# Performance work log

Hardware: AMD Instinct MI355X
Metric: run time of the kernel (lower is better)

Reference implementation:

```python
import jax, jax.numpy as jnp
import numpy as np

EMB = 1024
HEADS = 16
HEAD_DIM = EMB // HEADS
EPS = 1e-5


def gelu_tanh(x):
    c = jnp.sqrt(jnp.asarray(2.0 / jnp.pi, x.dtype))
    return 0.5 * x * (1 + jnp.tanh(c * (x + 0.044715 * x ** 3)))


def layernorm(x, scale, shift):
    mean = jnp.mean(x, axis=-1, keepdims=True)
    var = jnp.mean((x - mean) ** 2, axis=-1, keepdims=True)
    return scale * (x - mean) / jnp.sqrt(var + EPS) + shift


def setup_inputs() -> dict:
    key = jax.random.key(0)
    ks = jax.random.split(key, 12)
    s = 0.02
    x = jax.random.normal(ks[0], (2, 2048, EMB), dtype=jnp.float32)
    Wq = jax.random.normal(ks[1], (EMB, EMB), dtype=jnp.float32) * s
    Wk = jax.random.normal(ks[2], (EMB, EMB), dtype=jnp.float32) * s
    Wv = jax.random.normal(ks[3], (EMB, EMB), dtype=jnp.float32) * s
    Wo = jax.random.normal(ks[4], (EMB, EMB), dtype=jnp.float32) * s
    bo = jnp.zeros((EMB,), jnp.float32)
    W1 = jax.random.normal(ks[5], (EMB, 4 * EMB), dtype=jnp.float32) * s
    b1 = jnp.zeros((4 * EMB,), jnp.float32)
    W2 = jax.random.normal(ks[6], (4 * EMB, EMB), dtype=jnp.float32) * s
    b2 = jnp.zeros((EMB,), jnp.float32)
    g1 = jnp.ones((EMB,), jnp.float32)
    s1 = jnp.zeros((EMB,), jnp.float32)
    g2 = jnp.ones((EMB,), jnp.float32)
    s2 = jnp.zeros((EMB,), jnp.float32)
    return {"x": x, "Wq": Wq, "Wk": Wk, "Wv": Wv, "Wo": Wo, "bo": bo,
            "W1": W1, "b1": b1, "W2": W2, "b2": b2,
            "g1": g1, "s1": s1, "g2": g2, "s2": s2}


def reference(x, Wq, Wk, Wv, Wo, bo, W1, b1, W2, b2, g1, s1, g2, s2):
    B, S, D = x.shape
    # --- attention sub-block (pre-LN) ---
    h = layernorm(x, g1, s1)
    q = (h @ Wq).reshape(B, S, HEADS, HEAD_DIM).transpose(0, 2, 1, 3)
    k = (h @ Wk).reshape(B, S, HEADS, HEAD_DIM).transpose(0, 2, 1, 3)
    v = (h @ Wv).reshape(B, S, HEADS, HEAD_DIM).transpose(0, 2, 1, 3)
    scores = jnp.einsum('bhqd,bhkd->bhqk', q, k) / jnp.sqrt(
        jnp.asarray(HEAD_DIM, x.dtype))
    causal = jnp.triu(jnp.ones((S, S), bool), k=1)
    scores = jnp.where(causal, -jnp.inf, scores)
    attn = jax.nn.softmax(scores, axis=-1)
    ctx = jnp.einsum('bhqk,bhkd->bhqd', attn, v)
    ctx = ctx.transpose(0, 2, 1, 3).reshape(B, S, D)
    x = x + (ctx @ Wo + bo)
    # --- FFN sub-block (pre-LN) ---
    h = layernorm(x, g2, s2)
    h = gelu_tanh(h @ W1 + b1) @ W2 + b2
    return x + h
```

## Files before the change

kernel.cpp:

```cpp
#include <hip/hip_runtime.h>
#include <hip/hip_bf16.h>
#include <math.h>
#include <stdint.h>

typedef __bf16 bf16;
typedef __bf16 bf16x4 __attribute__((ext_vector_type(4)));
typedef __bf16 bf16x8 __attribute__((ext_vector_type(8)));
typedef float f32x4 __attribute__((ext_vector_type(4)));

#define MFMA16(a, b, c) __builtin_amdgcn_mfma_f32_16x16x32_bf16((a), (b), (c), 0, 0, 0)

constexpr int EMB = 1024;
constexpr int SEQ = 2048;
constexpr int BATCH = 2;
constexpr int NTOK = BATCH * SEQ;
constexpr int FFN = 4 * EMB;
constexpr int HEADS = 16;
constexpr int HDIM = 64;

#define QSCALE 0.18033688011112042f

__device__ __forceinline__ void gload16(const void* g, void* l) {
    __builtin_amdgcn_global_load_lds(
        (const __attribute__((address_space(1))) void*)g,
        (__attribute__((address_space(3))) void*)l,
        16, 0, 0);
}

__global__ __launch_bounds__(256) void ln_kernel(const float* __restrict__ x,
                                                 const float* __restrict__ g,
                                                 const float* __restrict__ b,
                                                 bf16* __restrict__ out) {
    int row = blockIdx.x;
    int t = threadIdx.x;
    float4 v = reinterpret_cast<const float4*>(x + (size_t)row * EMB)[t];
    float s = v.x + v.y + v.z + v.w;
    float s2 = v.x * v.x + v.y * v.y + v.z * v.z + v.w * v.w;
#pragma unroll
    for (int o = 1; o < 64; o <<= 1) {
        s += __shfl_xor(s, o);
        s2 += __shfl_xor(s2, o);
    }
    __shared__ float ps[4], ps2[4];
    int w = t >> 6;
    if ((t & 63) == 0) { ps[w] = s; ps2[w] = s2; }
    __syncthreads();
    s = ps[0] + ps[1] + ps[2] + ps[3];
    s2 = ps2[0] + ps2[1] + ps2[2] + ps2[3];
    float mean = s * (1.f / EMB);
    float var = s2 * (1.f / EMB) - mean * mean;
    float rstd = rsqrtf(var + 1e-5f);
    float4 gv = reinterpret_cast<const float4*>(g)[t];
    float4 bv = reinterpret_cast<const float4*>(b)[t];
    bf16* op = out + (size_t)row * EMB + t * 4;
    op[0] = (bf16)(gv.x * (v.x - mean) * rstd + bv.x);
    op[1] = (bf16)(gv.y * (v.y - mean) * rstd + bv.y);
    op[2] = (bf16)(gv.z * (v.z - mean) * rstd + bv.z);
    op[3] = (bf16)(gv.w * (v.w - mean) * rstd + bv.w);
}

__global__ __launch_bounds__(256) void transpose_all(
    const float* __restrict__ Wq, const float* __restrict__ Wk,
    const float* __restrict__ Wv, const float* __restrict__ Wo,
    const float* __restrict__ W1, const float* __restrict__ W2,
    bf16* __restrict__ Wqkvt, bf16* __restrict__ Wot,
    bf16* __restrict__ W1t, bf16* __restrict__ W2t) {
    int b = blockIdx.x;
    const float* W;
    bf16* Wt;
    int K, N, tile;
    if (b < 4096) {
        int w = b >> 10;
        tile = b & 1023;
        W = (w == 0) ? Wq : (w == 1) ? Wk : (w == 2) ? Wv : Wo;
        Wt = (w == 3) ? Wot : Wqkvt + (size_t)w * EMB * EMB;
        K = EMB; N = EMB;
    } else if (b < 8192) {
        tile = b - 4096; W = W1; Wt = W1t; K = EMB; N = FFN;
    } else {
        tile = b - 8192; W = W2; Wt = W2t; K = FFN; N = EMB;
    }
    int ntx = N / 32;
    int n0 = (tile % ntx) * 32, k0 = (tile / ntx) * 32;
    __shared__ float tl[32][33];
    int tx = threadIdx.x & 31, ty = threadIdx.x >> 5;
#pragma unroll
    for (int i = 0; i < 4; i++)
        tl[ty + 8 * i][tx] = W[(size_t)(k0 + ty + 8 * i) * N + n0 + tx];
    __syncthreads();
#pragma unroll
    for (int i = 0; i < 4; i++)
        Wt[(size_t)(n0 + ty + 8 * i) * K + k0 + tx] = (bf16)tl[tx][ty + 8 * i];
}

__global__ __launch_bounds__(256) void vtrans(const bf16* __restrict__ v,
                                              bf16* __restrict__ vt) {
    int bh = blockIdx.y;
    int s0 = blockIdx.x * 64;
    const bf16* src = v + (size_t)bh * SEQ * HDIM + (size_t)s0 * HDIM;
    bf16* dst = vt + (size_t)bh * HDIM * SEQ + s0;
    __shared__ bf16 tile[64][72];
    int t = threadIdx.x;
    int s = t >> 2, d0 = (t & 3) * 16;
    bf16x8 a = *reinterpret_cast<const bf16x8*>(src + s * HDIM + d0);
    bf16x8 b = *reinterpret_cast<const bf16x8*>(src + s * HDIM + d0 + 8);
#pragma unroll
    for (int e = 0; e < 8; e++) {
        tile[d0 + e][s] = a[e];
        tile[d0 + 8 + e][s] = b[e];
    }
    __syncthreads();
    int d = t >> 2, c0 = (t & 3) * 16;
    bf16x8 o0 = *reinterpret_cast<const bf16x8*>(&tile[d][c0]);
    bf16x8 o1 = *reinterpret_cast<const bf16x8*>(&tile[d][c0 + 8]);
    *reinterpret_cast<bf16x8*>(dst + (size_t)d * SEQ + c0) = o0;
    *reinterpret_cast<bf16x8*>(dst + (size_t)d * SEQ + c0 + 8) = o1;
}

template <int MODE>
__global__ __launch_bounds__(512, 1) void gemm8p(const bf16* __restrict__ A,
                                                 const bf16* __restrict__ Bt,
                                                 int K, int N,
                                                 bf16* __restrict__ outB,
                                                 bf16* __restrict__ outB2,
                                                 const float* __restrict__ bias) {
    extern __shared__ char smem[];
    int t = threadIdx.x;
    int wave = t >> 6, lane = t & 63;
    int wr = wave >> 2, wc = wave & 3;
    int lr = lane & 15, lg = lane >> 4;
    int row0 = blockIdx.x * 256;
    int col0 = blockIdx.y * 256;

    int tilesAll = K / 64;
    int nz = gridDim.z, z = blockIdx.z;
    int base = tilesAll / nz, rem = tilesAll - base * nz;
    int myT = base + (z < rem ? 1 : 0);
    int tBeg = z * base + (z < rem ? z : rem);

    const char* aSrc[4];
    const char* bSrc[4];
#pragma unroll
    for (int i = 0; i < 4; i++) {
        int f = t + i * 512;
        int gr = f >> 3, gk = f & 7;
        aSrc[i] = (const char*)A + ((size_t)(row0 + gr) * K + ((gk ^ (gr & 7)) << 3)) * 2
                  + (size_t)tBeg * 128;
        bSrc[i] = (const char*)Bt + ((size_t)(col0 + gr) * K + ((gk ^ (gr & 7)) << 3)) * 2
                  + (size_t)tBeg * 128;
    }

    f32x4 acc[8][4];
#pragma unroll
    for (int m = 0; m < 8; m++)
#pragma unroll
        for (int n = 0; n < 4; n++) acc[m][n] = f32x4{0.f, 0.f, 0.f, 0.f};

#pragma unroll
    for (int i = 0; i < 4; i++) {
        gload16(aSrc[i], smem + (t + i * 512) * 16);
        gload16(bSrc[i], smem + 32768 + (t + i * 512) * 16);
    }
    __syncthreads();

    for (int tk = 0; tk < myT; tk++) {
        int cur = tk & 1;
        const char* la = smem + cur * 65536;
        const char* lb = la + 32768;
        char* na = smem + (cur ^ 1) * 65536;
        bool stage = (tk + 1 < myT);

        bf16x8 bfr[2][4];
#pragma unroll
        for (int ph = 0; ph < 4; ph++) {
            constexpr int PH_KH[4] = {0, 0, 1, 1};
            constexpr int PH_MH[4] = {0, 1, 0, 1};
            const int kh = PH_KH[ph], mh = PH_MH[ph];
            bf16x8 afr[4];
#pragma unroll
            for (int m = 0; m < 4; m++) {
                int row = wr * 128 + (mh * 4 + m) * 16 + lr;
                int gk = kh * 4 + lg;
                afr[m] = *reinterpret_cast<const bf16x8*>(
                    la + row * 128 + ((gk ^ (row & 7)) << 4));
            }
            if (mh == 0) {
#pragma unroll
                for (int n = 0; n < 4; n++) {
                    int row = wc * 64 + n * 16 + lr;
                    int gk = kh * 4 + lg;
                    bfr[kh][n] = *reinterpret_cast<const bf16x8*>(
                        lb + row * 128 + ((gk ^ (row & 7)) << 4));
                }
            }
            if (stage) {
                gload16(aSrc[ph] + 128, na + (t + ph * 512) * 16);
                gload16(bSrc[ph] + 128, na + 32768 + (t + ph * 512) * 16);
            }
            __builtin_amdgcn_s_barrier();
            __builtin_amdgcn_s_setprio(1);
#pragma unroll
            for (int m = 0; m < 4; m++)
#pragma unroll
                for (int n = 0; n < 4; n++)
                    acc[mh * 4 + m][n] = MFMA16(afr[m], bfr[kh][n], acc[mh * 4 + m][n]);
            __builtin_amdgcn_s_setprio(0);
            __builtin_amdgcn_s_barrier();
        }
#pragma unroll
        for (int i = 0; i < 4; i++) { aSrc[i] += 128; bSrc[i] += 128; }
        __syncthreads();
    }

    float bi[4];
    if (MODE == 2) {
#pragma unroll
        for (int n = 0; n < 4; n++) bi[n] = bias[col0 + wc * 64 + n * 16 + lr];
    }
    bf16* pd = outB;
    if (MODE == 3) pd = (z < 2) ? outB + (size_t)z * ((size_t)NTOK * EMB) : outB2;
#pragma unroll
    for (int mf = 0; mf < 8; mf++) {
#pragma unroll
        for (int r = 0; r < 4; r++) {
            int row = row0 + wr * 128 + mf * 16 + 4 * lg + r;
#pragma unroll
            for (int n = 0; n < 4; n++) {
                int col = col0 + wc * 64 + n * 16 + lr;
                float v = acc[mf][n][r];
                if (MODE == 0) {
                    int b_ = row >> 11, s_ = row & 2047;
                    int which = col >> 10, rem_ = col & 1023;
                    int h_ = rem_ >> 6, d_ = rem_ & 63;
                    float sc = (which == 0) ? QSCALE : 1.0f;
                    outB[(size_t)which * (NTOK * EMB) +
                         (((size_t)(b_ * HEADS + h_) * SEQ + s_) << 6) + d_] =
                        (bf16)(v * sc);
                } else if (MODE == 2) {
                    float u = v + bi[n];
                    float gl = 0.5f * u *
                               (1.f + tanhf(0.7978845608028654f *
                                            (u + 0.044715f * u * u * u)));
                    outB[(size_t)row * N + col] = (bf16)gl;
                } else {
                    pd[(size_t)row * N + col] = (bf16)v;
                }
            }
        }
    }
}

__global__ __launch_bounds__(256) void ffn2_reduce(const float* __restrict__ x1,
                                                   const bf16* __restrict__ p01,
                                                   const bf16* __restrict__ p2,
                                                   const float* __restrict__ bias,
                                                   float* __restrict__ out) {
    constexpr int UNITS = NTOK * EMB / 4;
    const bf16* p1 = p01 + (size_t)NTOK * EMB;
    for (int i = blockIdx.x * 256 + threadIdx.x; i < UNITS; i += gridDim.x * 256) {
        float4 r = reinterpret_cast<const float4*>(x1)[i];
        float4 bv = reinterpret_cast<const float4*>(bias)[i & (EMB / 4 - 1)];
        bf16x4 a0 = reinterpret_cast<const bf16x4*>(p01)[i];
        bf16x4 a1 = reinterpret_cast<const bf16x4*>(p1)[i];
        bf16x4 a2 = reinterpret_cast<const bf16x4*>(p2)[i];
        r.x += (float)a0[0] + (float)a1[0] + (float)a2[0] + bv.x;
        r.y += (float)a0[1] + (float)a1[1] + (float)a2[1] + bv.y;
        r.z += (float)a0[2] + (float)a1[2] + (float)a2[2] + bv.z;
        r.w += (float)a0[3] + (float)a1[3] + (float)a2[3] + bv.w;
        reinterpret_cast<float4*>(out)[i] = r;
    }
}

template <int BM, int BN, int BK, int MODE>
__global__ __launch_bounds__(256) void gemm_lds(const bf16* __restrict__ A,
                                                const bf16* __restrict__ Bt,
                                                int M, int N, int K,
                                                float* __restrict__ outF,
                                                bf16* __restrict__ outB,
                                                const float* __restrict__ bias,
                                                const float* __restrict__ resid) {
    constexpr int MR = BM / 32;
    constexpr int NR = BN / 32;
    constexpr int ACH = (BM * BK * 2) / 4096;
    constexpr int BCH = (BN * BK * 2) / 4096;
    __shared__ bf16 sA[BM * BK];
    __shared__ bf16 sB[BN * BK];
    int t = threadIdx.x;
    int wave = t >> 6, lane = t & 63;
    int wr = wave >> 1, wc = wave & 1;
    int lr = lane & 15, lg = lane >> 4;
    int row0 = blockIdx.x * BM;
    int col0 = blockIdx.y * BN;

    const char* aS[ACH];
    const char* bS[BCH];
#pragma unroll
    for (int c = 0; c < ACH; c++) {
        int o = (t + c * 256) * 16;
        aS[c] = (const char*)A + (size_t)(row0 + o / (2 * BK)) * K * 2 + (o & (2 * BK - 1));
    }
#pragma unroll
    for (int c = 0; c < BCH; c++) {
        int o = (t + c * 256) * 16;
        bS[c] = (const char*)Bt + (size_t)(col0 + o / (2 * BK)) * K * 2 + (o & (2 * BK - 1));
    }

    f32x4 acc[MR][NR];
#pragma unroll
    for (int m = 0; m < MR; m++)
#pragma unroll
        for (int n = 0; n < NR; n++) acc[m][n] = f32x4{0.f, 0.f, 0.f, 0.f};

    for (int k0 = 0; k0 < K; k0 += BK) {
        __syncthreads();
#pragma unroll
        for (int c = 0; c < ACH; c++)
            gload16(aS[c], (char*)sA + (t + c * 256) * 16);
#pragma unroll
        for (int c = 0; c < BCH; c++)
            gload16(bS[c], (char*)sB + (t + c * 256) * 16);
#pragma unroll
        for (int c = 0; c < ACH; c++) aS[c] += 2 * BK;
#pragma unroll
        for (int c = 0; c < BCH; c++) bS[c] += 2 * BK;
        __syncthreads();

#pragma unroll
        for (int ks = 0; ks < BK / 32; ks++) {
            bf16x8 a[MR], b[NR];
#pragma unroll
            for (int m = 0; m < MR; m++)
                a[m] = *reinterpret_cast<const bf16x8*>(
                    sA + (wr * (BM / 2) + m * 16 + lr) * BK + ks * 32 + 8 * lg);
#pragma unroll
            for (int n = 0; n < NR; n++)
                b[n] = *reinterpret_cast<const bf16x8*>(
                    sB + (wc * (BN / 2) + n * 16 + lr) * BK + ks * 32 + 8 * lg);
#pragma unroll
            for (int m = 0; m < MR; m++)
#pragma unroll
                for (int n = 0; n < NR; n++)
                    acc[m][n] = MFMA16(a[m], b[n], acc[m][n]);
        }
    }

#pragma unroll
    for (int m = 0; m < MR; m++) {
#pragma unroll
        for (int r = 0; r < 4; r++) {
            int row = row0 + wr * (BM / 2) + m * 16 + 4 * lg + r;
#pragma unroll
            for (int n = 0; n < NR; n++) {
                int col = col0 + wc * (BN / 2) + n * 16 + lr;
                float v = acc[m][n][r];
                size_t idx = (size_t)row * N + col;
                outF[idx] = resid[idx] + v + bias[col];
            }
        }
    }
}

__global__ __launch_bounds__(256, 3) void attn_kernel(const bf16* __restrict__ q,
                                                      const bf16* __restrict__ k,
                                                      const bf16* __restrict__ vt,
                                                      bf16* __restrict__ ctx) {
    int wg = blockIdx.x;
    int wgid = (wg & 7) * 64 + (wg >> 3);
    int bh = wgid >> 4;
    int pair = wgid & 15;
    const bf16* qh = q + (size_t)bh * SEQ * HDIM;
    const bf16* kh = k + (size_t)bh * SEQ * HDIM;
    const bf16* vh = vt + (size_t)bh * HDIM * SEQ;
    int t = threadIdx.x;
    int wave = t >> 6, lane = t & 63;
    int lr = lane & 15, lg = lane >> 4;

    __shared__ bf16 sK[2][64 * 64];
    __shared__ bf16 sV[2][64 * 64];
    __shared__ bf16 plds[4][16][88];

    int grow = t >> 3, gg = t & 7;
    const bf16* kSrc0 = kh + (size_t)grow * HDIM + ((gg ^ (grow & 7)) << 3);
    const bf16* kSrc1 = kh + (size_t)(grow + 32) * HDIM + ((gg ^ ((grow + 32) & 7)) << 3);
    const bf16* vSrc0 = vh + (size_t)grow * SEQ + ((gg ^ (grow & 7)) << 3);
    const bf16* vSrc1 = vh + (size_t)(grow + 32) * SEQ + ((gg ^ ((grow + 32) & 7)) << 3);
    char* kD0 = (char*)&sK[0][0] + wave * 1024;
    char* vD0 = (char*)&sV[0][0] + wave * 1024;

    int swz = (lr & 7) << 4;
    int koff0 = (16 * lg) ^ swz;
    int koff1 = (64 + 16 * lg) ^ swz;
    int b_ = bh >> 4, h_ = bh & 15;

    for (int seg = 0; seg < 2; seg++) {
        int q0 = (seg == 0 ? (31 - pair) : pair) * 64;
        int qrow = q0 + wave * 16;

        bf16x8 qf0 = *reinterpret_cast<const bf16x8*>(
            qh + (size_t)(qrow + lr) * HDIM + 8 * lg);
        bf16x8 qf1 = *reinterpret_cast<const bf16x8*>(
            qh + (size_t)(qrow + lr) * HDIM + 32 + 8 * lg);

        f32x4 o[4];
#pragma unroll
        for (int n = 0; n < 4; n++) o[n] = f32x4{0.f, 0.f, 0.f, 0.f};
        float mx[4] = {-1e30f, -1e30f, -1e30f, -1e30f};
        float lsum[4] = {0.f, 0.f, 0.f, 0.f};

        int nc = q0 / 64 + 1;

        gload16(kSrc0, kD0);
        gload16(kSrc1, kD0 + 4096);
        gload16(vSrc0, vD0);
        gload16(vSrc1, vD0 + 4096);
        __syncthreads();

        for (int c = 0; c < nc; c++) {
            int c0 = c * 64;
            if (c + 1 < nc) {
                int nb = (c + 1) & 1;
                int cn = c0 + 64;
                gload16(kSrc0 + (size_t)cn * HDIM, kD0 + nb * 8192);
                gload16(kSrc1 + (size_t)cn * HDIM, kD0 + nb * 8192 + 4096);
                gload16(vSrc0 + cn, vD0 + nb * 8192);
                gload16(vSrc1 + cn, vD0 + nb * 8192 + 4096);
            }
            const char* kb_ = (const char*)&sK[c & 1][0];
            const char* vb_ = (const char*)&sV[c & 1][0];

            f32x4 st[4];
#pragma unroll
            for (int n = 0; n < 4; n++) {
                int ro = (16 * n + lr) * 128;
                bf16x8 kf0 = *reinterpret_cast<const bf16x8*>(kb_ + ro + koff0);
                bf16x8 kf1 = *reinterpret_cast<const bf16x8*>(kb_ + ro + koff1);
                f32x4 a = f32x4{0.f, 0.f, 0.f, 0.f};
                a = MFMA16(qf0, kf0, a);
                a = MFMA16(qf1, kf1, a);
                st[n] = a;
            }

            if (c0 == q0) {
#pragma unroll
                for (int n = 0; n < 4; n++)
#pragma unroll
                    for (int r = 0; r < 4; r++)
                        if (c0 + n * 16 + lr > qrow + 4 * lg + r) st[n][r] = -1e30f;
            }

            float mn[4], scl[4], ps[4];
#pragma unroll
            for (int r = 0; r < 4; r++) {
                float mp = fmaxf(fmaxf(st[0][r], st[1][r]), fmaxf(st[2][r], st[3][r]));
#pragma unroll
                for (int off = 1; off < 16; off <<= 1)
                    mp = fmaxf(mp, __shfl_xor(mp, off));
                mn[r] = fmaxf(mx[r], mp);
                scl[r] = __builtin_amdgcn_exp2f(mx[r] - mn[r]);
                mx[r] = mn[r];
                ps[r] = 0.f;
            }
#pragma unroll
            for (int n = 0; n < 4; n++)
#pragma unroll
                for (int r = 0; r < 4; r++) {
                    float p = __builtin_amdgcn_exp2f(st[n][r] - mn[r]);
                    ps[r] += p;
                    plds[wave][4 * lg + r][n * 16 + lr] = (bf16)p;
                }
#pragma unroll
            for (int r = 0; r < 4; r++) {
                float s = ps[r];
#pragma unroll
                for (int off = 1; off < 16; off <<= 1) s += __shfl_xor(s, off);
                lsum[r] = lsum[r] * scl[r] + s;
            }
#pragma unroll
            for (int n = 0; n < 4; n++) {
                o[n][0] *= scl[0]; o[n][1] *= scl[1];
                o[n][2] *= scl[2]; o[n][3] *= scl[3];
            }

#pragma unroll
            for (int ks = 0; ks < 2; ks++) {
                bf16x8 pa = *reinterpret_cast<const bf16x8*>(
                    &plds[wave][lr][ks * 32 + 8 * lg]);
                int vo = (64 * ks + 16 * lg) ^ swz;
#pragma unroll
                for (int n = 0; n < 4; n++) {
                    bf16x8 vf = *reinterpret_cast<const bf16x8*>(
                        vb_ + (16 * n + lr) * 128 + vo);
                    o[n] = MFMA16(pa, vf, o[n]);
                }
            }

            __syncthreads();
        }

#pragma unroll
        for (int r = 0; r < 4; r++) {
            float inv = 1.f / lsum[r];
            size_t base = ((size_t)b_ * SEQ + qrow + 4 * lg + r) * EMB + h_ * HDIM;
#pragma unroll
            for (int n = 0; n < 4; n++)
                ctx[base + n * 16 + lr] = (bf16)(o[n][r] * inv);
        }
    }
}

extern "C" void kernel_launch(void* const* d_in, const int* in_sizes, int n_in,
                              void* d_out, int out_size, void* d_ws, size_t ws_size,
                              hipStream_t stream) {
    const float* x  = (const float*)d_in[0];
    const float* Wq = (const float*)d_in[1];
    const float* Wk = (const float*)d_in[2];
    const float* Wv = (const float*)d_in[3];
    const float* Wo = (const float*)d_in[4];
    const float* bo = (const float*)d_in[5];
    const float* W1 = (const float*)d_in[6];
    const float* b1 = (const float*)d_in[7];
    const float* W2 = (const float*)d_in[8];
    const float* b2 = (const float*)d_in[9];
    const float* g1 = (const float*)d_in[10];
    const float* s1 = (const float*)d_in[11];
    const float* g2 = (const float*)d_in[12];
    const float* s2 = (const float*)d_in[13];

    const size_t MB = 1ull << 20;
    char* w = (char*)d_ws;
    bf16* Wqkvt = (bf16*)(w + 0 * MB);
    bf16* Wot = (bf16*)(w + 6 * MB);
    bf16* W1t = (bf16*)(w + 8 * MB);
    bf16* W2t = (bf16*)(w + 16 * MB);
    bf16* hbuf = (bf16*)(w + 24 * MB);
    bf16* vtb  = (bf16*)(w + 24 * MB);
    bf16* qkvb = (bf16*)(w + 32 * MB);
    bf16* qb   = (bf16*)(w + 32 * MB);
    bf16* kb   = (bf16*)(w + 40 * MB);
    bf16* vb   = (bf16*)(w + 48 * MB);
    bf16* ctxb = (bf16*)(w + 56 * MB);
    bf16* midb = (bf16*)(w + 32 * MB);
    float* x1  = (float*)(w + 64 * MB);
    bf16* p01  = (bf16*)(w + 0 * MB);
    bf16* p2   = (bf16*)(w + 24 * MB);

    hipFuncSetAttribute(reinterpret_cast<const void*>(gemm8p<0>),
                        hipFuncAttributeMaxDynamicSharedMemorySize, 131072);
    hipFuncSetAttribute(reinterpret_cast<const void*>(gemm8p<2>),
                        hipFuncAttributeMaxDynamicSharedMemorySize, 131072);
    hipFuncSetAttribute(reinterpret_cast<const void*>(gemm8p<3>),
                        hipFuncAttributeMaxDynamicSharedMemorySize, 131072);

    transpose_all<<<dim3(12288), 256, 0, stream>>>(Wq, Wk, Wv, Wo, W1, W2,
                                                   Wqkvt, Wot, W1t, W2t);

    ln_kernel<<<NTOK, 256, 0, stream>>>(x, g1, s1, hbuf);

    gemm8p<0><<<dim3(NTOK / 256, 3072 / 256), 512, 131072, stream>>>(
        hbuf, Wqkvt, EMB, 3072, qkvb, nullptr, nullptr);

    vtrans<<<dim3(SEQ / 64, BATCH * HEADS), 256, 0, stream>>>(vb, vtb);

    attn_kernel<<<dim3(512), 256, 0, stream>>>(qb, kb, vtb, ctxb);

    gemm_lds<128, 64, 32, 1><<<dim3(NTOK / 128, EMB / 64), 256, 0, stream>>>(
        ctxb, Wot, NTOK, EMB, EMB, x1, nullptr, bo, x);

    ln_kernel<<<NTOK, 256, 0, stream>>>(x1, g2, s2, hbuf);

    gemm8p<2><<<dim3(NTOK / 256, FFN / 256), 512, 131072, stream>>>(
        hbuf, W1t, EMB, FFN, midb, nullptr, b1);

    gemm8p<3><<<dim3(NTOK / 256, EMB / 256, 3), 512, 131072, stream>>>(
        midb, W2t, FFN, EMB, p01, p2, nullptr);
    ffn2_reduce<<<dim3(2048), 256, 0, stream>>>(x1, p01, p2, b2, (float*)d_out);
}
```

Measured before the change: 255.5 us.

## Process both causal query tiles concurrently in one 512-thread attention block

The attention kernel now uses 512 threads. The two paired query tiles (pair and 31-pair) are handled at the same time by the two halves of the block, instead of one after the other. Each K/V chunk is loaded into shared memory once and reused by both halves, and the early-finishing half simply idles through the remaining chunks. This removes the second pass's reloading of K/V chunks and the serial segment loop. In exchange, the shorter half's waves sit idle at the barriers, and the larger block may lower occupancy per CU.

```diff
diff --git a/kernel.cpp b/kernel.cpp
--- a/kernel.cpp
+++ b/kernel.cpp
@@ -360,7 +360,7 @@
     }
 }
 
-__global__ __launch_bounds__(256, 3) void attn_kernel(const bf16* __restrict__ q,
+__global__ __launch_bounds__(512, 2) void attn_kernel(const bf16* __restrict__ q,
                                                       const bf16* __restrict__ k,
                                                       const bf16* __restrict__ vt,
                                                       bf16* __restrict__ ctx) {
@@ -375,56 +375,52 @@
     int wave = t >> 6, lane = t & 63;
     int lr = lane & 15, lg = lane >> 4;
 
+    int half = wave >> 2;
+    int q0 = (half ? pair : (31 - pair)) * 64;
+    int qrow = q0 + (wave & 3) * 16;
+    int myNc = q0 / 64 + 1;
+    int ncAll = 32 - pair;
+
     __shared__ bf16 sK[2][64 * 64];
     __shared__ bf16 sV[2][64 * 64];
-    __shared__ bf16 plds[4][16][88];
+    __shared__ bf16 plds[8][16][88];
 
     int grow = t >> 3, gg = t & 7;
-    const bf16* kSrc0 = kh + (size_t)grow * HDIM + ((gg ^ (grow & 7)) << 3);
-    const bf16* kSrc1 = kh + (size_t)(grow + 32) * HDIM + ((gg ^ ((grow + 32) & 7)) << 3);
-    const bf16* vSrc0 = vh + (size_t)grow * SEQ + ((gg ^ (grow & 7)) << 3);
-    const bf16* vSrc1 = vh + (size_t)(grow + 32) * SEQ + ((gg ^ ((grow + 32) & 7)) << 3);
-    char* kD0 = (char*)&sK[0][0] + wave * 1024;
-    char* vD0 = (char*)&sV[0][0] + wave * 1024;
+    const bf16* kSrc = kh + (size_t)grow * HDIM + ((gg ^ (grow & 7)) << 3);
+    const bf16* vSrc = vh + (size_t)grow * SEQ + ((gg ^ (grow & 7)) << 3);
+    char* kD = (char*)&sK[0][0] + wave * 1024;
+    char* vD = (char*)&sV[0][0] + wave * 1024;
 
     int swz = (lr & 7) << 4;
     int koff0 = (16 * lg) ^ swz;
     int koff1 = (64 + 16 * lg) ^ swz;
     int b_ = bh >> 4, h_ = bh & 15;
 
-    for (int seg = 0; seg < 2; seg++) {
-        int q0 = (seg == 0 ? (31 - pair) : pair) * 64;
-        int qrow = q0 + wave * 16;
-
-        bf16x8 qf0 = *reinterpret_cast<const bf16x8*>(
-            qh + (size_t)(qrow + lr) * HDIM + 8 * lg);
-        bf16x8 qf1 = *reinterpret_cast<const bf16x8*>(
-            qh + (size_t)(qrow + lr) * HDIM + 32 + 8 * lg);
-
-        f32x4 o[4];
-#pragma unroll
-        for (int n = 0; n < 4; n++) o[n] = f32x4{0.f, 0.f, 0.f, 0.f};
-        float mx[4] = {-1e30f, -1e30f, -1e30f, -1e30f};
-        float lsum[4] = {0.f, 0.f, 0.f, 0.f};
-
-        int nc = q0 / 64 + 1;
-
-        gload16(kSrc0, kD0);
-        gload16(kSrc1, kD0 + 4096);
-        gload16(vSrc0, vD0);
-        gload16(vSrc1, vD0 + 4096);
-        __syncthreads();
-
-        for (int c = 0; c < nc; c++) {
-            int c0 = c * 64;
-            if (c + 1 < nc) {
-                int nb = (c + 1) & 1;
-                int cn = c0 + 64;
-                gload16(kSrc0 + (size_t)cn * HDIM, kD0 + nb * 8192);
-                gload16(kSrc1 + (size_t)cn * HDIM, kD0 + nb * 8192 + 4096);
-                gload16(vSrc0 + cn, vD0 + nb * 8192);
-                gload16(vSrc1 + cn, vD0 + nb * 8192 + 4096);
-            }
+    bf16x8 qf0 = *reinterpret_cast<const bf16x8*>(
+        qh + (size_t)(qrow + lr) * HDIM + 8 * lg);
+    bf16x8 qf1 = *reinterpret_cast<const bf16x8*>(
+        qh + (size_t)(qrow + lr) * HDIM + 32 + 8 * lg);
+
+    f32x4 o[4];
+#pragma unroll
+    for (int n = 0; n < 4; n++) o[n] = f32x4{0.f, 0.f, 0.f, 0.f};
+    float mx[4] = {-1e30f, -1e30f, -1e30f, -1e30f};
+    float lsum[4] = {0.f, 0.f, 0.f, 0.f};
+
+    gload16(kSrc, kD);
+    gload16(vSrc, vD);
+    __syncthreads();
+
+    for (int c = 0; c < ncAll; c++) {
+        int c0 = c * 64;
+        if (c + 1 < ncAll) {
+            int nb = (c + 1) & 1;
+            int cn = c0 + 64;
+            gload16(kSrc + (size_t)cn * HDIM, kD + nb * 8192);
+            gload16(vSrc + cn, vD + nb * 8192);
+        }
+
+        if (c < myNc) {
             const char* kb_ = (const char*)&sK[c & 1][0];
             const char* vb_ = (const char*)&sV[c & 1][0];
 
@@ -493,18 +489,18 @@
                     o[n] = MFMA16(pa, vf, o[n]);
                 }
             }
-
-            __syncthreads();
         }
 
-#pragma unroll
-        for (int r = 0; r < 4; r++) {
-            float inv = 1.f / lsum[r];
-            size_t base = ((size_t)b_ * SEQ + qrow + 4 * lg + r) * EMB + h_ * HDIM;
-#pragma unroll
-            for (int n = 0; n < 4; n++)
-                ctx[base + n * 16 + lr] = (bf16)(o[n][r] * inv);
-        }
+        __syncthreads();
+    }
+
+#pragma unroll
+    for (int r = 0; r < 4; r++) {
+        float inv = 1.f / lsum[r];
+        size_t base = ((size_t)b_ * SEQ + qrow + 4 * lg + r) * EMB + h_ * HDIM;
+#pragma unroll
+        for (int n = 0; n < 4; n++)
+            ctx[base + n * 16 + lr] = (bf16)(o[n][r] * inv);
     }
 }
 
@@ -561,7 +557,7 @@
 
     vtrans<<<dim3(SEQ / 64, BATCH * HEADS), 256, 0, stream>>>(vb, vtb);
 
-    attn_kernel<<<dim3(512), 256, 0, stream>>>(qb, kb, vtb, ctxb);
+    attn_kernel<<<dim3(512), 512, 0, stream>>>(qb, kb, vtb, ctxb);
 
     gemm_lds<128, 64, 32, 1><<<dim3(NTOK / 128, EMB / 64), 256, 0, stream>>>(
         ctxb, Wot, NTOK, EMB, EMB, x1, nullptr, bo, x);
```

Result: no change. 256.8 us (+0.5%).

## Rewrite attention with 32x32 MFMA, transposed scores, and single-pass paired query tiles

Applied to the files above, without the earlier changes.

The attention kernel moves from 16x16x32 to 32x32x16 bf16 MFMA and computes transposed score tiles (K as the A operand), so each lane owns one query row and the softmax reductions need only one cross-lane shuffle. The two sequential causal segments become one pass: waves 0-1 take the long query tile and waves 2-3 the short one, sharing a single K/V stream over the longer range. The goal is fewer instructions, less shuffle and LDS traffic per score, and reuse of shared K/V loads. In exchange, the short-tile waves sit idle for the remaining chunks while still hitting barriers, and 32x32 accumulators raise register pressure.

```diff
diff --git a/kernel.cpp b/kernel.cpp
--- a/kernel.cpp
+++ b/kernel.cpp
@@ -7,8 +7,10 @@
 typedef __bf16 bf16x4 __attribute__((ext_vector_type(4)));
 typedef __bf16 bf16x8 __attribute__((ext_vector_type(8)));
 typedef float f32x4 __attribute__((ext_vector_type(4)));
+typedef float f32x16 __attribute__((ext_vector_type(16)));
 
 #define MFMA16(a, b, c) __builtin_amdgcn_mfma_f32_16x16x32_bf16((a), (b), (c), 0, 0, 0)
+#define MFMA32(a, b, c) __builtin_amdgcn_mfma_f32_32x32x16_bf16((a), (b), (c), 0, 0, 0)
 
 constexpr int EMB = 1024;
 constexpr int SEQ = 2048;
@@ -373,11 +375,16 @@
     const bf16* vh = vt + (size_t)bh * HDIM * SEQ;
     int t = threadIdx.x;
     int wave = t >> 6, lane = t & 63;
-    int lr = lane & 15, lg = lane >> 4;
+    int ql = lane & 31, hi = lane >> 5;
+
+    int span = (wave < 2 ? (31 - pair) : pair) * 64;
+    int qrow = span + (wave & 1) * 32;
+    int myNc = span / 64 + 1;
+    int ncAll = 32 - pair;
 
     __shared__ bf16 sK[2][64 * 64];
     __shared__ bf16 sV[2][64 * 64];
-    __shared__ bf16 plds[4][16][88];
+    __shared__ bf16 plds[4][32][72];
 
     int grow = t >> 3, gg = t & 7;
     const bf16* kSrc0 = kh + (size_t)grow * HDIM + ((gg ^ (grow & 7)) << 3);
@@ -387,124 +394,116 @@
     char* kD0 = (char*)&sK[0][0] + wave * 1024;
     char* vD0 = (char*)&sV[0][0] + wave * 1024;
 
-    int swz = (lr & 7) << 4;
-    int koff0 = (16 * lg) ^ swz;
-    int koff1 = (64 + 16 * lg) ^ swz;
     int b_ = bh >> 4, h_ = bh & 15;
 
-    for (int seg = 0; seg < 2; seg++) {
-        int q0 = (seg == 0 ? (31 - pair) : pair) * 64;
-        int qrow = q0 + wave * 16;
-
-        bf16x8 qf0 = *reinterpret_cast<const bf16x8*>(
-            qh + (size_t)(qrow + lr) * HDIM + 8 * lg);
-        bf16x8 qf1 = *reinterpret_cast<const bf16x8*>(
-            qh + (size_t)(qrow + lr) * HDIM + 32 + 8 * lg);
-
-        f32x4 o[4];
-#pragma unroll
-        for (int n = 0; n < 4; n++) o[n] = f32x4{0.f, 0.f, 0.f, 0.f};
-        float mx[4] = {-1e30f, -1e30f, -1e30f, -1e30f};
-        float lsum[4] = {0.f, 0.f, 0.f, 0.f};
-
-        int nc = q0 / 64 + 1;
-
-        gload16(kSrc0, kD0);
-        gload16(kSrc1, kD0 + 4096);
-        gload16(vSrc0, vD0);
-        gload16(vSrc1, vD0 + 4096);
-        __syncthreads();
-
-        for (int c = 0; c < nc; c++) {
-            int c0 = c * 64;
-            if (c + 1 < nc) {
-                int nb = (c + 1) & 1;
-                int cn = c0 + 64;
-                gload16(kSrc0 + (size_t)cn * HDIM, kD0 + nb * 8192);
-                gload16(kSrc1 + (size_t)cn * HDIM, kD0 + nb * 8192 + 4096);
-                gload16(vSrc0 + cn, vD0 + nb * 8192);
-                gload16(vSrc1 + cn, vD0 + nb * 8192 + 4096);
-            }
+    bf16x8 qf[4];
+#pragma unroll
+    for (int ks = 0; ks < 4; ks++)
+        qf[ks] = *reinterpret_cast<const bf16x8*>(
+            qh + (size_t)(qrow + ql) * HDIM + ks * 16 + 8 * hi);
+
+    f32x16 o0, o1;
+#pragma unroll
+    for (int r = 0; r < 16; r++) { o0[r] = 0.f; o1[r] = 0.f; }
+    float mx = -1e30f, lsum = 0.f;
+
+    gload16(kSrc0, kD0);
+    gload16(kSrc1, kD0 + 4096);
+    gload16(vSrc0, vD0);
+    gload16(vSrc1, vD0 + 4096);
+    __syncthreads();
+
+    for (int c = 0; c < ncAll; c++) {
+        int c0 = c * 64;
+        if (c + 1 < ncAll) {
+            int nb = (c + 1) & 1;
+            int cn = c0 + 64;
+            gload16(kSrc0 + (size_t)cn * HDIM, kD0 + nb * 8192);
+            gload16(kSrc1 + (size_t)cn * HDIM, kD0 + nb * 8192 + 4096);
+            gload16(vSrc0 + cn, vD0 + nb * 8192);
+            gload16(vSrc1 + cn, vD0 + nb * 8192 + 4096);
+        }
+
+        if (c < myNc) {
             const char* kb_ = (const char*)&sK[c & 1][0];
             const char* vb_ = (const char*)&sV[c & 1][0];
 
-            f32x4 st[4];
-#pragma unroll
-            for (int n = 0; n < 4; n++) {
-                int ro = (16 * n + lr) * 128;
-                bf16x8 kf0 = *reinterpret_cast<const bf16x8*>(kb_ + ro + koff0);
-                bf16x8 kf1 = *reinterpret_cast<const bf16x8*>(kb_ + ro + koff1);
-                f32x4 a = f32x4{0.f, 0.f, 0.f, 0.f};
-                a = MFMA16(qf0, kf0, a);
-                a = MFMA16(qf1, kf1, a);
-                st[n] = a;
-            }
-
-            if (c0 == q0) {
-#pragma unroll
-                for (int n = 0; n < 4; n++)
-#pragma unroll
-                    for (int r = 0; r < 4; r++)
-                        if (c0 + n * 16 + lr > qrow + 4 * lg + r) st[n][r] = -1e30f;
-            }
-
-            float mn[4], scl[4], ps[4];
-#pragma unroll
-            for (int r = 0; r < 4; r++) {
-                float mp = fmaxf(fmaxf(st[0][r], st[1][r]), fmaxf(st[2][r], st[3][r]));
-#pragma unroll
-                for (int off = 1; off < 16; off <<= 1)
-                    mp = fmaxf(mp, __shfl_xor(mp, off));
-                mn[r] = fmaxf(mx[r], mp);
-                scl[r] = __builtin_amdgcn_exp2f(mx[r] - mn[r]);
-                mx[r] = mn[r];
-                ps[r] = 0.f;
-            }
-#pragma unroll
-            for (int n = 0; n < 4; n++)
-#pragma unroll
-                for (int r = 0; r < 4; r++) {
-                    float p = __builtin_amdgcn_exp2f(st[n][r] - mn[r]);
-                    ps[r] += p;
-                    plds[wave][4 * lg + r][n * 16 + lr] = (bf16)p;
+            f32x16 st0, st1;
+#pragma unroll
+            for (int r = 0; r < 16; r++) { st0[r] = 0.f; st1[r] = 0.f; }
+#pragma unroll
+            for (int ks = 0; ks < 4; ks++) {
+                int so = ((2 * ks + hi) ^ (ql & 7)) << 4;
+                bf16x8 kA0 = *reinterpret_cast<const bf16x8*>(kb_ + ql * 128 + so);
+                bf16x8 kA1 = *reinterpret_cast<const bf16x8*>(kb_ + (32 + ql) * 128 + so);
+                st0 = MFMA32(kA0, qf[ks], st0);
+                st1 = MFMA32(kA1, qf[ks], st1);
+            }
+
+            if (c == myNc - 1) {
+#pragma unroll
+                for (int r = 0; r < 16; r++) {
+                    int kl = c0 + (r & 3) + 8 * (r >> 2) + 4 * hi;
+                    if (kl > qrow + ql) st0[r] = -1e30f;
+                    if (kl + 32 > qrow + ql) st1[r] = -1e30f;
                 }
-#pragma unroll
-            for (int r = 0; r < 4; r++) {
-                float s = ps[r];
-#pragma unroll
-                for (int off = 1; off < 16; off <<= 1) s += __shfl_xor(s, off);
-                lsum[r] = lsum[r] * scl[r] + s;
-            }
-#pragma unroll
-            for (int n = 0; n < 4; n++) {
-                o[n][0] *= scl[0]; o[n][1] *= scl[1];
-                o[n][2] *= scl[2]; o[n][3] *= scl[3];
-            }
-
-#pragma unroll
-            for (int ks = 0; ks < 2; ks++) {
-                bf16x8 pa = *reinterpret_cast<const bf16x8*>(
-                    &plds[wave][lr][ks * 32 + 8 * lg]);
-                int vo = (64 * ks + 16 * lg) ^ swz;
-#pragma unroll
-                for (int n = 0; n < 4; n++) {
-                    bf16x8 vf = *reinterpret_cast<const bf16x8*>(
-                        vb_ + (16 * n + lr) * 128 + vo);
-                    o[n] = MFMA16(pa, vf, o[n]);
+            }
+
+            float pmax = -1e30f;
+#pragma unroll
+            for (int r = 0; r < 16; r++)
+                pmax = fmaxf(pmax, fmaxf(st0[r], st1[r]));
+            pmax = fmaxf(pmax, __shfl_xor(pmax, 32));
+            float mn = fmaxf(mx, pmax);
+            float scl = __builtin_amdgcn_exp2f(mx - mn);
+            mx = mn;
+            float ps = 0.f;
+#pragma unroll
+            for (int j = 0; j < 4; j++) {
+                bf16x4 w0, w1;
+#pragma unroll
+                for (int e = 0; e < 4; e++) {
+                    float p0 = __builtin_amdgcn_exp2f(st0[4 * j + e] - mn);
+                    float p1 = __builtin_amdgcn_exp2f(st1[4 * j + e] - mn);
+                    ps += p0 + p1;
+                    w0[e] = (bf16)p0;
+                    w1[e] = (bf16)p1;
                 }
-            }
-
-            __syncthreads();
-        }
-
-#pragma unroll
-        for (int r = 0; r < 4; r++) {
-            float inv = 1.f / lsum[r];
-            size_t base = ((size_t)b_ * SEQ + qrow + 4 * lg + r) * EMB + h_ * HDIM;
-#pragma unroll
-            for (int n = 0; n < 4; n++)
-                ctx[base + n * 16 + lr] = (bf16)(o[n][r] * inv);
-        }
+                *reinterpret_cast<bf16x4*>(&plds[wave][ql][8 * j + 4 * hi]) = w0;
+                *reinterpret_cast<bf16x4*>(&plds[wave][ql][32 + 8 * j + 4 * hi]) = w1;
+            }
+            ps += __shfl_xor(ps, 32);
+            lsum = lsum * scl + ps;
+#pragma unroll
+            for (int r = 0; r < 16; r++) { o0[r] *= scl; o1[r] *= scl; }
+
+#pragma unroll
+            for (int ks = 0; ks < 4; ks++) {
+                bf16x8 pb = *reinterpret_cast<const bf16x8*>(
+                    &plds[wave][ql][ks * 16 + 8 * hi]);
+                int so = ((2 * ks + hi) ^ (ql & 7)) << 4;
+                bf16x8 vA0 = *reinterpret_cast<const bf16x8*>(vb_ + ql * 128 + so);
+                bf16x8 vA1 = *reinterpret_cast<const bf16x8*>(vb_ + (32 + ql) * 128 + so);
+                o0 = MFMA32(vA0, pb, o0);
+                o1 = MFMA32(vA1, pb, o1);
+            }
+        }
+
+        __syncthreads();
+    }
+
+    float inv = 1.f / lsum;
+    size_t base = ((size_t)b_ * SEQ + qrow + ql) * EMB + h_ * HDIM;
+#pragma unroll
+    for (int j = 0; j < 4; j++) {
+        bf16x4 w0, w1;
+#pragma unroll
+        for (int e = 0; e < 4; e++) {
+            w0[e] = (bf16)(o0[4 * j + e] * inv);
+            w1[e] = (bf16)(o1[4 * j + e] * inv);
+        }
+        *reinterpret_cast<bf16x4*>(ctx + base + 8 * j + 4 * hi) = w0;
+        *reinterpret_cast<bf16x4*>(ctx + base + 32 + 8 * j + 4 * hi) = w1;
     }
 }
 
```

New measurement: 246.9 us. 1.03x faster.
